# Kernel tuning notes

Measured on AMD Instinct MI355X. Metric: run time of the kernel, lower is better.

## Reference

```python
import jax, jax.numpy as jnp
import numpy as np

B = 32            # batch size
N = 100           # n_nodes (== MAX_N_NODES here)
MAXN = 100        # MAX_N_NODES
H = 256           # HIDDEN_DIM_FEATURES_EXTRACTOR
HA = 1024         # HIDDEN_DIM_ACTOR
HC = 512          # HIDDEN_DIM_CRITIC
K_ACTIVE = 5000   # exact number of active mask entries per batch element


def setup_inputs() -> dict:
    key = jax.random.key(0)
    ks = jax.random.split(key, 16)
    feat = jax.random.normal(ks[0], (B, N + 1, H), jnp.float32)
    # mask: exactly K_ACTIVE ones among N*N per batch row (dim == K for all rows)
    rng = np.random.default_rng(0)
    mask = np.zeros((B, N * N), np.float32)
    for i in range(B):
        mask[i, rng.choice(N * N, size=K_ACTIVE, replace=False)] = 1.0
    mask = jnp.asarray(mask).reshape(B, N, N)
    ext_mask = jnp.concatenate([jnp.zeros((B, 1, N), jnp.float32), mask], axis=1)  # [B, N+1, N]
    embedded_features = jnp.concatenate([feat, ext_mask], axis=2)  # [B, N+1, H+N]

    def lin(k, fi, fo):
        s = 1.0 / np.sqrt(fi)
        return (jax.random.uniform(k, (fi, fo), jnp.float32, -s, s),
                jax.random.uniform(jax.random.fold_in(k, 1), (fo,), jnp.float32, -s, s))

    aW1, ab1 = lin(ks[1], 3 * H, HA)
    aW2, ab2 = lin(ks[2], HA, HA)
    aW3, ab3 = lin(ks[3], HA, 1)
    cW1, cb1 = lin(ks[4], H, HC)
    cW2, cb2 = lin(ks[5], HC, HC)
    cW3, cb3 = lin(ks[6], HC, 1)
    return dict(embedded_features=embedded_features,
                aW1=aW1, ab1=ab1, aW2=aW2, ab2=ab2, aW3=aW3, ab3=ab3,
                cW1=cW1, cb1=cb1, cW2=cW2, cb2=cb2, cW3=cW3, cb3=cb3,
                K=K_ACTIVE)


def reference(embedded_features, aW1, ab1, aW2, ab2, aW3, ab3,
              cW1, cb1, cW2, cb2, cW3, cb3, K):
    # decompose features
    gn = embedded_features[:, :, :H]
    ext_mask = embedded_features[:, :, H:]
    g = gn[:, :1, :]                      # [B,1,H] graph embedding
    nodes = gn[:, 1:, :]                  # [B,N,H] node embeddings
    mask = ext_mask[:, 1:, :].reshape(B, -1)  # [B, N*N]

    # indexes of active pairs (stable top_k -> ascending indices among ones, like nonzero)
    _, idx = jax.lax.top_k(mask, K)       # [B,K] int32
    idx1 = idx // N
    idx2 = idx % N
    n1 = jnp.take_along_axis(nodes, idx1[:, :, None], axis=1)  # [B,K,H]
    n2 = jnp.take_along_axis(nodes, idx2[:, :, None], axis=1)  # [B,K,H]
    pairs = jnp.concatenate([jnp.broadcast_to(g, (B, K, H)), n1, n2], axis=-1)  # [B,K,3H]

    # actor MLP (tanh hidden activations)
    h = jnp.tanh(pairs @ aW1 + ab1)
    h = jnp.tanh(h @ aW2 + ab2)
    logits = h @ aW3 + ab3                # [B,K,1]
    pi = jax.nn.softmax(logits, axis=1)   # softmax over the K gathered pairs

    # scatter back into padded grid
    shaped = jnp.zeros((B, N * N), pi.dtype).at[jnp.arange(B)[:, None], idx].set(pi[..., 0])
    filled = jnp.zeros((B, MAXN, MAXN), pi.dtype).at[:, :N, :N].set(shaped.reshape(B, N, N))
    filled = filled.reshape(B, MAXN * MAXN)

    # critic MLP on graph embedding
    hv = jnp.tanh(g @ cW1 + cb1)
    hv = jnp.tanh(hv @ cW2 + cb2)
    value = hv @ cW3 + cb3                # [B,1,1]
    return filled, value
```

## Files before the change

kernel.cpp:

```cpp
#include <hip/hip_runtime.h>
#include <stdint.h>

#define AS1 __attribute__((address_space(1)))
#define AS3 __attribute__((address_space(3)))

typedef __bf16 bf16x8 __attribute__((ext_vector_type(8)));
typedef float  f32x4  __attribute__((ext_vector_type(4)));
typedef int    i32x4  __attribute__((ext_vector_type(4)));
typedef int    i32x8  __attribute__((ext_vector_type(8)));
typedef float  f32x16 __attribute__((ext_vector_type(16)));

__device__ __forceinline__ float tanh_fast(float x){
    float e = __expf(2.0f * x);
    return 1.0f - 2.0f * __builtin_amdgcn_rcpf(e + 1.0f);
}
__device__ __forceinline__ float tanh4_fast(float x){
    float e = __expf(2.0f * x);
    return fmaf(-8.0f, __builtin_amdgcn_rcpf(e + 1.0f), 4.0f);
}

__device__ __forceinline__ unsigned short f2bf(float f){
    unsigned int u = __float_as_uint(f);
    u = (u + 0x7fffu + ((u >> 16) & 1u)) >> 16;
    return (unsigned short)u;
}

template<int SEL>
__device__ __forceinline__ unsigned int pk4(unsigned int old, float a, float b){
#if defined(__has_builtin) && __has_builtin(__builtin_amdgcn_cvt_scalef32_pk_fp4_f32)
    return __builtin_amdgcn_cvt_scalef32_pk_fp4_f32(old, a, b, 1.0f, SEL);
#else
    float fa = fabsf(a), fb = fabsf(b);
    unsigned int ma = fa < 0.25f ? 0u : fa < 0.75f ? 1u : fa < 1.25f ? 2u :
                      fa < 1.75f ? 3u : fa < 2.5f  ? 4u : fa < 3.5f  ? 5u :
                      fa < 5.0f  ? 6u : 7u;
    unsigned int mb = fb < 0.25f ? 0u : fb < 0.75f ? 1u : fb < 1.25f ? 2u :
                      fb < 1.75f ? 3u : fb < 2.5f  ? 4u : fb < 3.5f  ? 5u :
                      fb < 5.0f  ? 6u : 7u;
    ma |= (a < 0.0f ? 8u : 0u); mb |= (b < 0.0f ? 8u : 0u);
    return old | ((ma | (mb << 4)) << (8 * SEL));
#endif
}

__device__ __forceinline__ i32x8 lo4(i32x4 a){
    return __builtin_shufflevector(a, a, 0, 1, 2, 3, -1, -1, -1, -1);
}

#define B2F(u, lo, hi) { lo = __uint_as_float((u) << 16); hi = __uint_as_float((u) & 0xffff0000u); }

__global__ __launch_bounds__(256) void k_stage1(
    const float* __restrict__ ef,  const float* __restrict__ aW1, const float* __restrict__ ab1,
    const float* __restrict__ aW2,
    const float* __restrict__ cW1, const float* __restrict__ cb1,
    const float* __restrict__ cW2, const float* __restrict__ cb2,
    const float* __restrict__ cW3, const float* __restrict__ cb3,
    int* __restrict__ pairs, unsigned char* __restrict__ w2b,
    unsigned short* __restrict__ P, float* __restrict__ out, int* __restrict__ qctr)
{
    int blk = blockIdx.x;
    int t = threadIdx.x;
    __shared__ __align__(16) unsigned short an[112 * 264];
    __shared__ float gsh[256], gpart[4][64];
    __shared__ int s_base, s_woff[4], s_wc[4];
    __shared__ float gs[256], h1[512], h2[512], wred[4];

    if (blk == 512 && t == 0) qctr[0] = 0;

    if (blk < 512){
        int cb = blk & 15, b = blk >> 4;
        for (int e = t; e < 25600; e += 256){
            int row = e >> 8, col = e & 255;
            an[row * 264 + col] = f2bf(ef[(size_t)b * 35956 + (size_t)(1 + row) * 356 + col]);
        }
        for (int e = t; e < 3168; e += 256) an[26400 + e] = 0;
        gsh[t] = ef[(size_t)b * 35956 + t];
        __syncthreads();

        {
            int cl = t & 63, q = t >> 6;
            const float* a1p = aW1 + (size_t)(q * 64) * 1024 + cb * 64 + cl;
            float p = 0.f;
            for (int i = 0; i < 64; ++i) p += gsh[q * 64 + i] * a1p[(size_t)i * 1024];
            gpart[q][cl] = p;
        }
        __syncthreads();

        int w = t >> 6, lane = t & 63, quad = lane >> 4, n = lane & 15;
        int c = cb * 64 + w * 16 + n;
        bf16x8 bfr0[8], bfr1[8];
        const float* wp0 = aW1 + (size_t)(256 + quad * 8) * 1024 + c;
        const float* wp1 = aW1 + (size_t)(512 + quad * 8) * 1024 + c;
#pragma unroll
        for (int kt = 0; kt < 8; ++kt){
            unsigned int w0[4], w1[4];
#pragma unroll
            for (int jj = 0; jj < 4; ++jj){
                size_t off0 = (size_t)(kt * 32 + 2 * jj) * 1024;
                size_t off1 = off0 + 1024;
                w0[jj] = (unsigned int)f2bf(wp0[off0]) | ((unsigned int)f2bf(wp0[off1]) << 16);
                w1[jj] = (unsigned int)f2bf(wp1[off0]) | ((unsigned int)f2bf(wp1[off1]) << 16);
            }
            uint4 p0 = make_uint4(w0[0], w0[1], w0[2], w0[3]);
            uint4 p1 = make_uint4(w1[0], w1[1], w1[2], w1[3]);
            bfr0[kt] = *(bf16x8*)&p0;
            bfr1[kt] = *(bf16x8*)&p1;
        }
        f32x4 acc0[7], acc1[7];
#pragma unroll
        for (int m = 0; m < 7; ++m){ f32x4 z = {0.f, 0.f, 0.f, 0.f}; acc0[m] = z; acc1[m] = z; }
#pragma unroll
        for (int kt = 0; kt < 8; ++kt){
#pragma unroll
            for (int m = 0; m < 7; ++m){
                const bf16x8* ap = (const bf16x8*)(an + (m * 16 + n) * 264 + kt * 32 + quad * 8);
                bf16x8 av = *ap;
                acc0[m] = __builtin_amdgcn_mfma_f32_16x16x32_bf16(av, bfr0[kt], acc0[m], 0, 0, 0);
                acc1[m] = __builtin_amdgcn_mfma_f32_16x16x32_bf16(av, bfr1[kt], acc1[m], 0, 0, 0);
            }
        }
        int cw = w * 16 + n;
        float addv = gpart[0][cw] + gpart[1][cw] + gpart[2][cw] + gpart[3][cw] + ab1[c];
        size_t base = (size_t)b * 102400;
#pragma unroll
        for (int m = 0; m < 7; ++m){
            int r0 = m * 16 + quad * 4;
#pragma unroll
            for (int r = 0; r < 4; ++r){
                int row = r0 + r;
                if (row < 100){
                    P[base + (size_t)row * 1024 + c]           = f2bf(acc0[m][r] + addv);
                    P[3276800 + base + (size_t)row * 1024 + c] = f2bf(acc1[m][r]);
                }
            }
        }
    } else if (blk < 544){
        int b = blk - 512;
        if (t == 0) s_base = 0;
        __syncthreads();
        int lane = t & 63, w = t >> 6;
        for (int ch = 0; ch < 40; ++ch){
            int pos = ch * 256 + t;
            bool valid = false;
            if (pos < 10000){
                int r = pos / 100, c = pos - (pos / 100) * 100;
                valid = ef[(size_t)b * 35956 + (size_t)(1 + r) * 356 + 256 + c] != 0.0f;
            }
            unsigned long long bal = __ballot(valid);
            if (lane == 0) s_wc[w] = __popcll(bal);
            __syncthreads();
            if (t == 0){
                int r = s_base;
                for (int q = 0; q < 4; ++q){ s_woff[q] = r; r += s_wc[q]; }
                s_base = r;
            }
            __syncthreads();
            if (valid){
                int rank = __popcll(bal & ((1ull << lane) - 1ull));
                int o = s_woff[w] + rank;
                if (o < 5000) pairs[b * 5000 + o] = pos;
            }
            __syncthreads();
        }
    } else if (blk < 672){
        int tid = (blk - 544) * 256 + t;
        int lane = tid & 63, kt = (tid >> 6) & 15, ct = tid >> 10;
        int lh = lane >> 5, n = lane & 31;
        const float* src = aW2 + (size_t)(kt * 64 + lh * 32) * 1024 + ct * 32 + n;
        unsigned int d[4] = {0u, 0u, 0u, 0u};
#pragma unroll
        for (int j = 0; j < 32; ++j){
            float a = src[(size_t)j * 1024] * 128.0f;
            float f = fabsf(a);
            unsigned int m = f < 0.25f ? 0u : f < 0.75f ? 1u : f < 1.25f ? 2u :
                             f < 1.75f ? 3u : f < 2.5f  ? 4u : f < 3.5f  ? 5u :
                             f < 5.0f  ? 6u : 7u;
            unsigned int nib = m | (a < 0.0f ? 8u : 0u);
            d[j >> 3] |= nib << (4 * (j & 7));
        }
        *(uint4*)(w2b + (size_t)(ct * 16 + kt) * 1024 + lane * 16) =
            make_uint4(d[0], d[1], d[2], d[3]);
    } else {
        int b = blk - 672;
        gs[t] = ef[(size_t)b * 35956 + t];
        __syncthreads();
        for (int o = t; o < 512; o += 256){
            float a = cb1[o];
            for (int i = 0; i < 256; ++i) a += gs[i] * cW1[(size_t)i * 512 + o];
            h1[o] = tanh_fast(a);
        }
        __syncthreads();
        for (int o = t; o < 512; o += 256){
            float a = cb2[o];
            for (int i = 0; i < 512; ++i) a += h1[i] * cW2[(size_t)i * 512 + o];
            h2[o] = tanh_fast(a);
        }
        __syncthreads();
        float p = h2[t] * cW3[t] + h2[t + 256] * cW3[t + 256];
        for (int m = 32; m >= 1; m >>= 1) p += __shfl_xor(p, m);
        if ((t & 63) == 0) wred[t >> 6] = p;
        __syncthreads();
        if (t == 0) out[320000 + b] = wred[0] + wred[1] + wred[2] + wred[3] + cb3[0];
    }
}

__global__ __launch_bounds__(256, 4) void k_main(
    const int* __restrict__ pairs,
    const unsigned short* __restrict__ P1, const unsigned short* __restrict__ P2,
    const unsigned char* __restrict__ w2b, const float* __restrict__ ab2,
    const float* __restrict__ aW3, float* __restrict__ logits, int* __restrict__ qctr)
{
    __shared__ __align__(16) unsigned char wbuf[2][16384];
    __shared__ int s_tile;
    int t = threadIdx.x, w = t >> 6, lane = t & 63;
    int lrow = lane & 31, lh = lane >> 5;
    int soff = w * 4096 + lane * 16;

    for (;;){
        if (t == 0) s_tile = atomicAdd(qctr, 1);
        __syncthreads();
        int tt = s_tile;
        if (tt >= 1280) break;
        int b = tt / 40, tile = tt - b * 40;

        {
            const unsigned char* s = w2b + soff;
            unsigned char* d = &wbuf[0][0] + soff;
#pragma unroll
            for (int i = 0; i < 4; ++i)
                __builtin_amdgcn_global_load_lds((AS1 void*)(s + i * 1024),
                                                 (AS3 void*)(d + i * 1024), 16, 0, 0);
        }

        int grow = tile * 128 + w * 32 + lrow;
        int pidx = pairs[b * 5000 + (grow < 5000 ? grow : 4999)];
        int i1 = pidx / 100, i2 = pidx - i1 * 100;
        const uint4* pa = (const uint4*)(P1 + (((size_t)(b * 100 + i1)) << 10)) + lh * 4;
        const uint4* pb = (const uint4*)(P2 + (((size_t)(b * 100 + i2)) << 10)) + lh * 4;

        i32x4 af4[16];
#pragma unroll
        for (int kt = 0; kt < 16; ++kt){
            uint4 qa[4], qb[4];
#pragma unroll
            for (int j = 0; j < 4; ++j){ qa[j] = pa[kt * 8 + j]; qb[j] = pb[kt * 8 + j]; }
            unsigned int d[4];
#pragma unroll
            for (int j = 0; j < 4; ++j){
                float a0, a1, b0, b1;
                unsigned int dd = 0;
                B2F(qa[j].x, a0, a1); B2F(qb[j].x, b0, b1);
                dd = pk4<0>(dd, tanh4_fast(a0 + b0), tanh4_fast(a1 + b1));
                B2F(qa[j].y, a0, a1); B2F(qb[j].y, b0, b1);
                dd = pk4<1>(dd, tanh4_fast(a0 + b0), tanh4_fast(a1 + b1));
                B2F(qa[j].z, a0, a1); B2F(qb[j].z, b0, b1);
                dd = pk4<2>(dd, tanh4_fast(a0 + b0), tanh4_fast(a1 + b1));
                B2F(qa[j].w, a0, a1); B2F(qb[j].w, b0, b1);
                dd = pk4<3>(dd, tanh4_fast(a0 + b0), tanh4_fast(a1 + b1));
                d[j] = dd;
            }
            i32x4 f = {(int)d[0], (int)d[1], (int)d[2], (int)d[3]};
            af4[kt] = f;
        }

        float prt[16];
#pragma unroll
        for (int r = 0; r < 16; ++r) prt[r] = 0.f;
        f32x16 acc;

        for (int ct = 0; ct < 32; ++ct){
            __syncthreads();
            if (ct < 31){
                const unsigned char* sp = w2b + (size_t)(ct + 1) * 16384 + soff;
                unsigned char* d = &wbuf[(ct + 1) & 1][0] + soff;
#pragma unroll
                for (int i = 0; i < 4; ++i)
                    __builtin_amdgcn_global_load_lds((AS1 void*)(sp + i * 1024),
                                                     (AS3 void*)(d + i * 1024), 16, 0, 0);
            }
#pragma unroll
            for (int r = 0; r < 16; ++r) acc[r] = 0.f;
            const unsigned char* bb = &wbuf[ct & 1][0] + lane * 16;
#pragma unroll
            for (int kt = 0; kt < 16; ++kt){
                uint4 q = *(const uint4*)(bb + kt * 1024);
                i32x4 bq = {(int)q.x, (int)q.y, (int)q.z, (int)q.w};
                acc = __builtin_amdgcn_mfma_scale_f32_32x32x64_f8f6f4(
                          lo4(af4[kt]), lo4(bq), acc, 4, 4, 0, 0x7D7D7D7D, 0, 0x78787878);
            }
            int c = ct * 32 + lrow;
            float w3 = aW3[c], bias = ab2[c];
#pragma unroll
            for (int r = 0; r < 16; ++r)
                prt[r] += tanh_fast(acc[r] + bias) * w3;
        }

#pragma unroll
        for (int r = 0; r < 16; ++r){
            float v = prt[r];
            v += __shfl_xor(v, 1); v += __shfl_xor(v, 2); v += __shfl_xor(v, 4);
            v += __shfl_xor(v, 8); v += __shfl_xor(v, 16);
            if (lrow == 0){
                int row = (r & 3) + 8 * (r >> 2) + 4 * lh;
                int g = tile * 128 + w * 32 + row;
                if (g < 5000) logits[b * 5000 + g] = v;
            }
        }
    }
}

__global__ void k_soft(const float* __restrict__ logits, const int* __restrict__ pairs,
                       float* __restrict__ out){
    int b = blockIdx.x, t = threadIdx.x;
    __shared__ float red[4];
    __shared__ float bmS, bsS;
    float* ob = out + (size_t)b * 10000;
    for (int j = t; j < 10000; j += 256) ob[j] = 0.0f;
    const float* lg = logits + b * 5000;
    float m = -1e30f;
    for (int j = t; j < 5000; j += 256) m = fmaxf(m, lg[j]);
    for (int s = 32; s >= 1; s >>= 1) m = fmaxf(m, __shfl_xor(m, s));
    if ((t & 63) == 0) red[t >> 6] = m;
    __syncthreads();
    if (t == 0) bmS = fmaxf(fmaxf(red[0], red[1]), fmaxf(red[2], red[3]));
    __syncthreads();
    float mm = bmS;
    float s = 0.f;
    for (int j = t; j < 5000; j += 256) s += __expf(lg[j] - mm);
    for (int k = 32; k >= 1; k >>= 1) s += __shfl_xor(s, k);
    if ((t & 63) == 0) red[t >> 6] = s;
    __syncthreads();
    if (t == 0) bsS = 1.0f / (red[0] + red[1] + red[2] + red[3]);
    __syncthreads();
    float inv = bsS;
    for (int j = t; j < 5000; j += 256){
        int pos = pairs[b * 5000 + j];
        ob[pos] = __expf(lg[j] - mm) * inv;
    }
}

extern "C" void kernel_launch(void* const* d_in, const int* in_sizes, int n_in,
                              void* d_out, int out_size, void* d_ws, size_t ws_size,
                              hipStream_t stream) {
    (void)in_sizes; (void)n_in; (void)out_size; (void)ws_size;
    const float* ef  = (const float*)d_in[0];
    const float* aW1 = (const float*)d_in[1];
    const float* ab1 = (const float*)d_in[2];
    const float* aW2 = (const float*)d_in[3];
    const float* ab2 = (const float*)d_in[4];
    const float* aW3 = (const float*)d_in[5];
    const float* cW1 = (const float*)d_in[7];
    const float* cb1 = (const float*)d_in[8];
    const float* cW2 = (const float*)d_in[9];
    const float* cb2 = (const float*)d_in[10];
    const float* cW3 = (const float*)d_in[11];
    const float* cb3 = (const float*)d_in[12];
    float* out = (float*)d_out;
    char* ws = (char*)d_ws;
    int*   pairs  = (int*)(ws + 0);
    float* logits = (float*)(ws + 640000);
    unsigned short* P1 = (unsigned short*)(ws + 1411072);
    unsigned short* P2 = (unsigned short*)(ws + 7964672);
    unsigned char*  w2b = (unsigned char*)(ws + 14518272);
    int*   qctr   = (int*)(ws + 16615424);

    k_stage1<<<704,  256, 0, stream>>>(ef, aW1, ab1, aW2, cW1, cb1, cW2, cb2, cW3, cb3,
                                       pairs, w2b, P1, out, qctr);
    k_main  <<<1024, 256, 0, stream>>>(pairs, P1, P2, w2b, ab2, aW3, logits, qctr);
    k_soft  <<<32,   256, 0, stream>>>(logits, pairs, out);
}
```

Measured before the change: 311.0 us.

## Split stage1 into weight-prep and GEMM kernels, cheapen tanh and fp4 quantization

Adds a stage0 kernel that converts the aW1 node weights to bf16 once and computes the graph-embedding projection once per batch. Stage1 then loads the pre-packed weights with vector loads instead of having each of its 512 blocks reconvert fp32 weights. Other changes: hardware packed bf16 conversion, atomics instead of barriers for pair compaction, a piecewise-linear approximation replacing tanh before fp4 quantization, and a tanh-via-exp2 rewrite that folds the constant term out of the loop. This adds an extra kernel launch and a dependency between stage0 and stage1, and the piecewise approximation may change the quantized values.

```diff
diff --git a/kernel.cpp b/kernel.cpp
--- a/kernel.cpp
+++ b/kernel.cpp
@@ -14,15 +14,31 @@
     float e = __expf(2.0f * x);
     return 1.0f - 2.0f * __builtin_amdgcn_rcpf(e + 1.0f);
 }
-__device__ __forceinline__ float tanh4_fast(float x){
-    float e = __expf(2.0f * x);
-    return fmaf(-8.0f, __builtin_amdgcn_rcpf(e + 1.0f), 4.0f);
-}
-
-__device__ __forceinline__ unsigned short f2bf(float f){
-    unsigned int u = __float_as_uint(f);
-    u = (u + 0x7fffu + ((u >> 16) & 1u)) >> 16;
-    return (unsigned short)u;
+
+__device__ __forceinline__ unsigned int cvt_pk_bf16(float lo, float hi){
+    unsigned int r;
+    asm("v_cvt_pk_bf16_f32 %0, %1, %2" : "=v"(r) : "v"(lo), "v"(hi));
+    return r;
+}
+__device__ __forceinline__ unsigned short f2bf1(float f){
+    return (unsigned short)(cvt_pk_bf16(f, f) & 0xffffu);
+}
+
+__device__ __forceinline__ float exp2_fast(float x){
+#if defined(__has_builtin) && __has_builtin(__builtin_amdgcn_exp2f)
+    return __builtin_amdgcn_exp2f(x);
+#else
+    float r; asm("v_exp_f32 %0, %1" : "=v"(r) : "v"(x)); return r;
+#endif
+}
+
+__device__ __forceinline__ float q4s(float s){
+    float a  = fabsf(s);
+    float m1 = fmaf(a, 3.931945f, 0.0039260f);
+    float m2 = fmaf(a, 3.428853f, 0.1414056f);
+    float m3 = fmaf(a, 1.610679f, 1.3191011f);
+    float g  = fminf(fminf(m1, m2), fminf(m3, 4.0f));
+    return __builtin_copysignf(g, s);
 }
 
 template<int SEL>
@@ -48,121 +64,74 @@
 
 #define B2F(u, lo, hi) { lo = __uint_as_float((u) << 16); hi = __uint_as_float((u) & 0xffff0000u); }
 
-__global__ __launch_bounds__(256) void k_stage1(
-    const float* __restrict__ ef,  const float* __restrict__ aW1, const float* __restrict__ ab1,
+__global__ __launch_bounds__(256) void k_stage0(
+    const float* __restrict__ ef, const float* __restrict__ aW1, const float* __restrict__ ab1,
     const float* __restrict__ aW2,
     const float* __restrict__ cW1, const float* __restrict__ cb1,
     const float* __restrict__ cW2, const float* __restrict__ cb2,
     const float* __restrict__ cW3, const float* __restrict__ cb3,
+    unsigned short* __restrict__ w1b, float* __restrict__ g1,
     int* __restrict__ pairs, unsigned char* __restrict__ w2b,
-    unsigned short* __restrict__ P, float* __restrict__ out, int* __restrict__ qctr)
+    float* __restrict__ out, int* __restrict__ qctr)
 {
-    int blk = blockIdx.x;
-    int t = threadIdx.x;
-    __shared__ __align__(16) unsigned short an[112 * 264];
-    __shared__ float gsh[256], gpart[4][64];
-    __shared__ int s_base, s_woff[4], s_wc[4];
-    __shared__ float gs[256], h1[512], h2[512], wred[4];
-
-    if (blk == 512 && t == 0) qctr[0] = 0;
-
-    if (blk < 512){
-        int cb = blk & 15, b = blk >> 4;
-        for (int e = t; e < 25600; e += 256){
-            int row = e >> 8, col = e & 255;
-            an[row * 264 + col] = f2bf(ef[(size_t)b * 35956 + (size_t)(1 + row) * 356 + col]);
-        }
-        for (int e = t; e < 3168; e += 256) an[26400 + e] = 0;
-        gsh[t] = ef[(size_t)b * 35956 + t];
-        __syncthreads();
-
-        {
-            int cl = t & 63, q = t >> 6;
-            const float* a1p = aW1 + (size_t)(q * 64) * 1024 + cb * 64 + cl;
-            float p = 0.f;
-            for (int i = 0; i < 64; ++i) p += gsh[q * 64 + i] * a1p[(size_t)i * 1024];
-            gpart[q][cl] = p;
-        }
-        __syncthreads();
-
+    __shared__ float gsl[256];
+    __shared__ float h1[512], h2[512], wred[4];
+    __shared__ int lcnt;
+    int blk = blockIdx.x, t = threadIdx.x;
+    if (blk == 0 && t == 0) qctr[0] = 0;
+
+    if (blk < 256){
+        int s = blk >> 7, cb = (blk >> 3) & 15, kt = blk & 7;
         int w = t >> 6, lane = t & 63, quad = lane >> 4, n = lane & 15;
         int c = cb * 64 + w * 16 + n;
-        bf16x8 bfr0[8], bfr1[8];
-        const float* wp0 = aW1 + (size_t)(256 + quad * 8) * 1024 + c;
-        const float* wp1 = aW1 + (size_t)(512 + quad * 8) * 1024 + c;
-#pragma unroll
-        for (int kt = 0; kt < 8; ++kt){
-            unsigned int w0[4], w1[4];
-#pragma unroll
-            for (int jj = 0; jj < 4; ++jj){
-                size_t off0 = (size_t)(kt * 32 + 2 * jj) * 1024;
-                size_t off1 = off0 + 1024;
-                w0[jj] = (unsigned int)f2bf(wp0[off0]) | ((unsigned int)f2bf(wp0[off1]) << 16);
-                w1[jj] = (unsigned int)f2bf(wp1[off0]) | ((unsigned int)f2bf(wp1[off1]) << 16);
-            }
-            uint4 p0 = make_uint4(w0[0], w0[1], w0[2], w0[3]);
-            uint4 p1 = make_uint4(w1[0], w1[1], w1[2], w1[3]);
-            bfr0[kt] = *(bf16x8*)&p0;
-            bfr1[kt] = *(bf16x8*)&p1;
-        }
-        f32x4 acc0[7], acc1[7];
-#pragma unroll
-        for (int m = 0; m < 7; ++m){ f32x4 z = {0.f, 0.f, 0.f, 0.f}; acc0[m] = z; acc1[m] = z; }
-#pragma unroll
-        for (int kt = 0; kt < 8; ++kt){
-#pragma unroll
-            for (int m = 0; m < 7; ++m){
-                const bf16x8* ap = (const bf16x8*)(an + (m * 16 + n) * 264 + kt * 32 + quad * 8);
-                bf16x8 av = *ap;
-                acc0[m] = __builtin_amdgcn_mfma_f32_16x16x32_bf16(av, bfr0[kt], acc0[m], 0, 0, 0);
-                acc1[m] = __builtin_amdgcn_mfma_f32_16x16x32_bf16(av, bfr1[kt], acc1[m], 0, 0, 0);
-            }
-        }
-        int cw = w * 16 + n;
-        float addv = gpart[0][cw] + gpart[1][cw] + gpart[2][cw] + gpart[3][cw] + ab1[c];
-        size_t base = (size_t)b * 102400;
-#pragma unroll
-        for (int m = 0; m < 7; ++m){
-            int r0 = m * 16 + quad * 4;
-#pragma unroll
-            for (int r = 0; r < 4; ++r){
-                int row = r0 + r;
-                if (row < 100){
-                    P[base + (size_t)row * 1024 + c]           = f2bf(acc0[m][r] + addv);
-                    P[3276800 + base + (size_t)row * 1024 + c] = f2bf(acc1[m][r]);
-                }
-            }
-        }
-    } else if (blk < 544){
-        int b = blk - 512;
-        if (t == 0) s_base = 0;
-        __syncthreads();
-        int lane = t & 63, w = t >> 6;
-        for (int ch = 0; ch < 40; ++ch){
-            int pos = ch * 256 + t;
+        const float* src = aW1 + (size_t)(256 + s * 256 + kt * 32 + quad * 8) * 1024 + c;
+        unsigned int d[4];
+#pragma unroll
+        for (int j = 0; j < 4; ++j)
+            d[j] = cvt_pk_bf16(src[(size_t)(2*j) * 1024], src[(size_t)(2*j+1) * 1024]);
+        *(uint4*)(w1b + (size_t)blk * 2048 + t * 8) = make_uint4(d[0], d[1], d[2], d[3]);
+    } else if (blk < 288){
+        int b = blk - 256;
+        gsl[t] = ef[(size_t)b * 35956 + t];
+        __syncthreads();
+        float s0 = 0.f, s1 = 0.f, s2 = 0.f, s3 = 0.f;
+#pragma unroll 4
+        for (int i = 0; i < 256; ++i){
+            float gv = gsl[i];
+            const float* r = aW1 + (size_t)i * 1024 + t;
+            s0 = fmaf(gv, r[0],   s0);
+            s1 = fmaf(gv, r[256], s1);
+            s2 = fmaf(gv, r[512], s2);
+            s3 = fmaf(gv, r[768], s3);
+        }
+        float* gb = g1 + b * 1024 + t;
+        gb[0]   = s0 + ab1[t];
+        gb[256] = s1 + ab1[t + 256];
+        gb[512] = s2 + ab1[t + 512];
+        gb[768] = s3 + ab1[t + 768];
+    } else if (blk < 320){
+        int b = blk - 288;
+        int lane = t & 63;
+        if (t == 0) lcnt = 0;
+        __syncthreads();
+        for (int i = 0; i < 40; ++i){
+            int pos = i * 256 + t;
             bool valid = false;
             if (pos < 10000){
-                int r = pos / 100, c = pos - (pos / 100) * 100;
-                valid = ef[(size_t)b * 35956 + (size_t)(1 + r) * 356 + 256 + c] != 0.0f;
+                int r = pos / 100, cc = pos - r * 100;
+                valid = ef[(size_t)b * 35956 + (size_t)(1 + r) * 356 + 256 + cc] != 0.0f;
             }
             unsigned long long bal = __ballot(valid);
-            if (lane == 0) s_wc[w] = __popcll(bal);
-            __syncthreads();
-            if (t == 0){
-                int r = s_base;
-                for (int q = 0; q < 4; ++q){ s_woff[q] = r; r += s_wc[q]; }
-                s_base = r;
-            }
-            __syncthreads();
+            int wbase;
+            if (lane == 0) wbase = atomicAdd(&lcnt, __popcll(bal));
+            wbase = __shfl(wbase, 0);
             if (valid){
-                int rank = __popcll(bal & ((1ull << lane) - 1ull));
-                int o = s_woff[w] + rank;
-                if (o < 5000) pairs[b * 5000 + o] = pos;
-            }
-            __syncthreads();
-        }
-    } else if (blk < 672){
-        int tid = (blk - 544) * 256 + t;
+                int o = wbase + __popcll(bal & ((1ull << lane) - 1ull));
+                pairs[b * 5000 + o] = pos;
+            }
+        }
+    } else if (blk < 448){
+        int tid = (blk - 320) * 256 + t;
         int lane = tid & 63, kt = (tid >> 6) & 15, ct = tid >> 10;
         int lh = lane >> 5, n = lane & 31;
         const float* src = aW2 + (size_t)(kt * 64 + lh * 32) * 1024 + ct * 32 + n;
@@ -180,17 +149,19 @@
         *(uint4*)(w2b + (size_t)(ct * 16 + kt) * 1024 + lane * 16) =
             make_uint4(d[0], d[1], d[2], d[3]);
     } else {
-        int b = blk - 672;
-        gs[t] = ef[(size_t)b * 35956 + t];
+        int b = blk - 448;
+        gsl[t] = ef[(size_t)b * 35956 + t];
         __syncthreads();
         for (int o = t; o < 512; o += 256){
             float a = cb1[o];
-            for (int i = 0; i < 256; ++i) a += gs[i] * cW1[(size_t)i * 512 + o];
+#pragma unroll 4
+            for (int i = 0; i < 256; ++i) a += gsl[i] * cW1[(size_t)i * 512 + o];
             h1[o] = tanh_fast(a);
         }
         __syncthreads();
         for (int o = t; o < 512; o += 256){
             float a = cb2[o];
+#pragma unroll 4
             for (int i = 0; i < 512; ++i) a += h1[i] * cW2[(size_t)i * 512 + o];
             h2[o] = tanh_fast(a);
         }
@@ -200,6 +171,64 @@
         if ((t & 63) == 0) wred[t >> 6] = p;
         __syncthreads();
         if (t == 0) out[320000 + b] = wred[0] + wred[1] + wred[2] + wred[3] + cb3[0];
+    }
+}
+
+__global__ __launch_bounds__(256) void k_stage1(
+    const float* __restrict__ ef, const unsigned short* __restrict__ w1b,
+    const float* __restrict__ g1, unsigned short* __restrict__ P)
+{
+    __shared__ __align__(16) unsigned short an[112 * 264];
+    int blk = blockIdx.x, t = threadIdx.x;
+    int cb = blk & 15, b = blk >> 4;
+
+    for (int it = 0; it < 25; ++it){
+        int idx = it * 256 + t;
+        int row = idx >> 6, c4 = idx & 63;
+        const float* sp = ef + (size_t)b * 35956 + (size_t)(1 + row) * 356 + c4 * 4;
+        float4 f = *(const float4*)sp;
+        *(uint2*)(an + row * 264 + c4 * 4) =
+            make_uint2(cvt_pk_bf16(f.x, f.y), cvt_pk_bf16(f.z, f.w));
+    }
+    for (int e = t; e < 3168; e += 256) an[26400 + e] = 0;
+    __syncthreads();
+
+    int w = t >> 6, lane = t & 63, quad = lane >> 4, n = lane & 15;
+    int c = cb * 64 + w * 16 + n;
+    bf16x8 bfr0[8], bfr1[8];
+#pragma unroll
+    for (int kt = 0; kt < 8; ++kt){
+        uint4 q0 = *(const uint4*)(w1b + ((size_t)(      cb * 8 + kt) * 256 + t) * 8);
+        uint4 q1 = *(const uint4*)(w1b + ((size_t)(128 + cb * 8 + kt) * 256 + t) * 8);
+        bfr0[kt] = *(bf16x8*)&q0;
+        bfr1[kt] = *(bf16x8*)&q1;
+    }
+    f32x4 acc0[7], acc1[7];
+#pragma unroll
+    for (int m = 0; m < 7; ++m){ f32x4 z = {0.f, 0.f, 0.f, 0.f}; acc0[m] = z; acc1[m] = z; }
+#pragma unroll
+    for (int kt = 0; kt < 8; ++kt){
+#pragma unroll
+        for (int m = 0; m < 7; ++m){
+            const bf16x8* ap = (const bf16x8*)(an + (m * 16 + n) * 264 + kt * 32 + quad * 8);
+            bf16x8 av = *ap;
+            acc0[m] = __builtin_amdgcn_mfma_f32_16x16x32_bf16(av, bfr0[kt], acc0[m], 0, 0, 0);
+            acc1[m] = __builtin_amdgcn_mfma_f32_16x16x32_bf16(av, bfr1[kt], acc1[m], 0, 0, 0);
+        }
+    }
+    float addv = g1[b * 1024 + c];
+    size_t base = (size_t)b * 102400;
+#pragma unroll
+    for (int m = 0; m < 7; ++m){
+        int r0 = m * 16 + quad * 4;
+#pragma unroll
+        for (int r = 0; r < 4; ++r){
+            int row = r0 + r;
+            if (row < 100){
+                P[base + (size_t)row * 1024 + c]           = f2bf1(acc0[m][r] + addv);
+                P[3276800 + base + (size_t)row * 1024 + c] = f2bf1(acc1[m][r]);
+            }
+        }
     }
 }
 
@@ -249,13 +278,13 @@
                 float a0, a1, b0, b1;
                 unsigned int dd = 0;
                 B2F(qa[j].x, a0, a1); B2F(qb[j].x, b0, b1);
-                dd = pk4<0>(dd, tanh4_fast(a0 + b0), tanh4_fast(a1 + b1));
+                dd = pk4<0>(dd, q4s(a0 + b0), q4s(a1 + b1));
                 B2F(qa[j].y, a0, a1); B2F(qb[j].y, b0, b1);
-                dd = pk4<1>(dd, tanh4_fast(a0 + b0), tanh4_fast(a1 + b1));
+                dd = pk4<1>(dd, q4s(a0 + b0), q4s(a1 + b1));
                 B2F(qa[j].z, a0, a1); B2F(qb[j].z, b0, b1);
-                dd = pk4<2>(dd, tanh4_fast(a0 + b0), tanh4_fast(a1 + b1));
+                dd = pk4<2>(dd, q4s(a0 + b0), q4s(a1 + b1));
                 B2F(qa[j].w, a0, a1); B2F(qb[j].w, b0, b1);
-                dd = pk4<3>(dd, tanh4_fast(a0 + b0), tanh4_fast(a1 + b1));
+                dd = pk4<3>(dd, q4s(a0 + b0), q4s(a1 + b1));
                 d[j] = dd;
             }
             i32x4 f = {(int)d[0], (int)d[1], (int)d[2], (int)d[3]};
@@ -265,6 +294,7 @@
         float prt[16];
 #pragma unroll
         for (int r = 0; r < 16; ++r) prt[r] = 0.f;
+        float sw3 = 0.f;
         f32x16 acc;
 
         for (int ct = 0; ct < 32; ++ct){
@@ -287,16 +317,22 @@
                 acc = __builtin_amdgcn_mfma_scale_f32_32x32x64_f8f6f4(
                           lo4(af4[kt]), lo4(bq), acc, 4, 4, 0, 0x7D7D7D7D, 0, 0x78787878);
             }
-            int c = ct * 32 + lrow;
-            float w3 = aW3[c], bias = ab2[c];
-#pragma unroll
-            for (int r = 0; r < 16; ++r)
-                prt[r] += tanh_fast(acc[r] + bias) * w3;
+            int cc = ct * 32 + lrow;
+            float w3  = aW3[cc];
+            float bc  = ab2[cc] * 2.8853900817779268f;
+            float w3m = -2.0f * w3;
+            sw3 += w3;
+#pragma unroll
+            for (int r = 0; r < 16; ++r){
+                float a = fmaf(acc[r], 2.8853900817779268f, bc);
+                float e = exp2_fast(a);
+                prt[r] = fmaf(w3m, __builtin_amdgcn_rcpf(e + 1.0f), prt[r]);
+            }
         }
 
 #pragma unroll
         for (int r = 0; r < 16; ++r){
-            float v = prt[r];
+            float v = prt[r] + sw3;
             v += __shfl_xor(v, 1); v += __shfl_xor(v, 2); v += __shfl_xor(v, 4);
             v += __shfl_xor(v, 8); v += __shfl_xor(v, 16);
             if (lrow == 0){
@@ -361,10 +397,13 @@
     unsigned short* P1 = (unsigned short*)(ws + 1411072);
     unsigned short* P2 = (unsigned short*)(ws + 7964672);
     unsigned char*  w2b = (unsigned char*)(ws + 14518272);
+    unsigned short* w1b = (unsigned short*)(ws + 15042560);
+    float* g1     = (float*)(ws + 16091136);
     int*   qctr   = (int*)(ws + 16615424);
 
-    k_stage1<<<704,  256, 0, stream>>>(ef, aW1, ab1, aW2, cW1, cb1, cW2, cb2, cW3, cb3,
-                                       pairs, w2b, P1, out, qctr);
+    k_stage0<<<480,  256, 0, stream>>>(ef, aW1, ab1, aW2, cW1, cb1, cW2, cb2, cW3, cb3,
+                                       w1b, g1, pairs, w2b, out, qctr);
+    k_stage1<<<512,  256, 0, stream>>>(ef, w1b, g1, P1);
     k_main  <<<1024, 256, 0, stream>>>(pairs, P1, P2, w2b, ab2, aW3, logits, qctr);
     k_soft  <<<32,   256, 0, stream>>>(logits, pairs, out);
 }
```

Measured after the change: 385.1 us. +23.8%, slower.
